# Optimization experiments

Hardware: AMD Instinct MI355X
Metric: run time of the kernel (lower is better)

Reference implementation:

```python
import jax, jax.numpy as jnp
import numpy as np

EMBED_DIM = 1024
HIDDEN = 128
N_QUERY = 65536
N_PROTO = 512


def setup_inputs() -> dict:
    key = jax.random.key(0)
    k1, k2, k3, k4, k5, k6, k7 = jax.random.split(key, 7)
    d2 = EMBED_DIM * 2
    lim1 = 1.0 / np.sqrt(d2)
    lim2 = 1.0 / np.sqrt(HIDDEN)
    return {
        "query_features": jax.random.normal(k1, (N_QUERY, EMBED_DIM), dtype=jnp.float32),
        "prototypes": jax.random.normal(k2, (N_PROTO, EMBED_DIM), dtype=jnp.float32),
        "distances": jax.random.uniform(k3, (N_QUERY, N_PROTO), dtype=jnp.float32),
        "W1": jax.random.uniform(k4, (d2, HIDDEN), minval=-lim1, maxval=lim1, dtype=jnp.float32),
        "b1": jax.random.uniform(k5, (HIDDEN,), minval=-lim1, maxval=lim1, dtype=jnp.float32),
        "W2": jax.random.uniform(k6, (HIDDEN, 1), minval=-lim2, maxval=lim2, dtype=jnp.float32),
        "b2": jax.random.uniform(k7, (1,), minval=-lim2, maxval=lim2, dtype=jnp.float32),
    }


def reference(query_features, prototypes, distances, W1, b1, W2, b2):
    # Batched version of the per-query loop: argmin -> gather -> concat -> MLP.
    idx = jnp.argmin(distances, axis=1)                      # [N_QUERY]
    closest = prototypes[idx]                                # [N_QUERY, D]
    combined = jnp.concatenate([query_features, closest], axis=-1)  # [N_QUERY, 2D]
    h = jax.nn.relu(combined @ W1 + b1)                      # [N_QUERY, 128]
    out = jax.nn.sigmoid(h @ W2 + b2)                        # [N_QUERY, 1]
    return jnp.squeeze(out, axis=-1)                         # [N_QUERY]
```

## Files before the change

kernel.cpp:

```cpp
#include <hip/hip_runtime.h>
#include <math.h>

#define EMBED 1024
#define HIDDEN 128
#define NPROTO 512

typedef short bf16x8 __attribute__((ext_vector_type(8)));
typedef float f32x4 __attribute__((ext_vector_type(4)));

__device__ __forceinline__ unsigned short f2bf(float x) {
    unsigned u = __builtin_bit_cast(unsigned, x);
    unsigned r = u + 0x7FFFu + ((u >> 16) & 1u);
    return (unsigned short)(r >> 16);
}

__global__ __launch_bounds__(256) void prep_kernel(
    const float* __restrict__ prototypes,
    const float* __restrict__ W1,
    float* __restrict__ proto_h,
    unsigned short* __restrict__ w1t)
{
    int b = blockIdx.x;
    int t = threadIdx.x;
    if (b < 256) {
        int ph = t >> 7, h = t & 127;
        int p = b * 2 + ph;
        const float* pr = prototypes + (size_t)p * EMBED;
        const float* w  = W1 + (size_t)EMBED * HIDDEN + h;
        float acc = 0.f;
        for (int k = 0; k < EMBED; k += 8) {
            #pragma unroll
            for (int j = 0; j < 8; ++j)
                acc += pr[k + j] * w[(size_t)(k + j) * HIDDEN];
        }
        proto_h[(size_t)p * HIDDEN + h] = acc;
    } else {
        int s = (b - 256) * 256 + t;
        int n = s & 127;
        int k0 = (s >> 7) * 8;
        bf16x8 v;
        #pragma unroll
        for (int j = 0; j < 8; ++j)
            v[j] = (short)f2bf(W1[(size_t)(k0 + j) * HIDDEN + n]);
        *(bf16x8*)(w1t + (size_t)n * EMBED + k0) = v;
    }
}

__global__ __launch_bounds__(256, 2) void main_kernel(
    const float* __restrict__ qf,
    const float* __restrict__ dist,
    const float* __restrict__ b1,
    const float* __restrict__ W2,
    const float* __restrict__ b2,
    const float* __restrict__ proto_h,
    const unsigned short* __restrict__ w1t,
    float* __restrict__ out)
{
    __shared__ int s_idx[4][32];

    const int t = threadIdx.x;
    const int wave = t >> 6, lane = t & 63;
    const int quad = lane >> 4, tid16 = lane & 15;
    const int q0 = blockIdx.x * 128 + wave * 32;

    const float* abase = qf + (size_t)(q0 + tid16) * EMBED + quad * 8;
    const unsigned short* bbase = w1t + (size_t)tid16 * EMBED + quad * 8;

    float4 aA[2][2], aB[2][2];
    #pragma unroll
    for (int mi = 0; mi < 2; ++mi) {
        const float* p = abase + (size_t)(mi * 16) * EMBED;
        aA[mi][0] = *(const float4*)(p);
        aA[mi][1] = *(const float4*)(p + 4);
        aB[mi][0] = *(const float4*)(p + 32);
        aB[mi][1] = *(const float4*)(p + 36);
    }

    for (int i = 0; i < 32; i += 4) {
        float4 v0[4], v1[4];
        #pragma unroll
        for (int j = 0; j < 4; ++j) {
            const float* dr = dist + (size_t)(q0 + i + j) * NPROTO;
            v0[j] = ((const float4*)dr)[lane];
            v1[j] = ((const float4*)dr)[lane + 64];
        }
        #pragma unroll
        for (int j = 0; j < 4; ++j) {
            float bv = v0[j].x; int bi = lane * 4;
            if (v0[j].y < bv) { bv = v0[j].y; bi = lane * 4 + 1; }
            if (v0[j].z < bv) { bv = v0[j].z; bi = lane * 4 + 2; }
            if (v0[j].w < bv) { bv = v0[j].w; bi = lane * 4 + 3; }
            int c = 256 + lane * 4;
            if (v1[j].x < bv) { bv = v1[j].x; bi = c; }
            if (v1[j].y < bv) { bv = v1[j].y; bi = c + 1; }
            if (v1[j].z < bv) { bv = v1[j].z; bi = c + 2; }
            if (v1[j].w < bv) { bv = v1[j].w; bi = c + 3; }
            #pragma unroll
            for (int s = 1; s < 64; s <<= 1) {
                float ov = __shfl_xor(bv, s);
                int   oi = __shfl_xor(bi, s);
                if (ov < bv || (ov == bv && oi < bi)) { bv = ov; bi = oi; }
            }
            if (lane == 0) s_idx[wave][i + j] = bi;
        }
    }

    f32x4 acc[2][8];
    #pragma unroll
    for (int mi = 0; mi < 2; ++mi)
        #pragma unroll
        for (int ni = 0; ni < 8; ++ni)
            acc[mi][ni] = (f32x4){0.f, 0.f, 0.f, 0.f};

#define LOAD_A(dst, kk)                                              \
    do {                                                             \
        _Pragma("unroll")                                            \
        for (int mi = 0; mi < 2; ++mi) {                             \
            const float* p = abase + (size_t)(mi * 16) * EMBED + (kk) * 32; \
            dst[mi][0] = *(const float4*)(p);                        \
            dst[mi][1] = *(const float4*)(p + 4);                    \
        }                                                            \
    } while (0)

#define CVT_A(af, src)                                               \
    do {                                                             \
        _Pragma("unroll")                                            \
        for (int mi = 0; mi < 2; ++mi) {                             \
            af[mi][0] = (short)f2bf(src[mi][0].x);                   \
            af[mi][1] = (short)f2bf(src[mi][0].y);                   \
            af[mi][2] = (short)f2bf(src[mi][0].z);                   \
            af[mi][3] = (short)f2bf(src[mi][0].w);                   \
            af[mi][4] = (short)f2bf(src[mi][1].x);                   \
            af[mi][5] = (short)f2bf(src[mi][1].y);                   \
            af[mi][6] = (short)f2bf(src[mi][1].z);                   \
            af[mi][7] = (short)f2bf(src[mi][1].w);                   \
        }                                                            \
    } while (0)

    for (int k = 0; k < 32; k += 2) {
        {
            bf16x8 bfr[8];
            #pragma unroll
            for (int ni = 0; ni < 8; ++ni)
                bfr[ni] = *(const bf16x8*)(bbase + (size_t)(ni * 16) * EMBED + k * 32);
            bf16x8 af[2];
            CVT_A(af, aA);
            if (k + 2 < 32) LOAD_A(aA, k + 2);
            #pragma unroll
            for (int mi = 0; mi < 2; ++mi)
                #pragma unroll
                for (int ni = 0; ni < 8; ++ni)
                    acc[mi][ni] = __builtin_amdgcn_mfma_f32_16x16x32_bf16(
                        af[mi], bfr[ni], acc[mi][ni], 0, 0, 0);
        }
        {
            bf16x8 bfr[8];
            #pragma unroll
            for (int ni = 0; ni < 8; ++ni)
                bfr[ni] = *(const bf16x8*)(bbase + (size_t)(ni * 16) * EMBED + (k + 1) * 32);
            bf16x8 af[2];
            CVT_A(af, aB);
            if (k + 3 < 32) LOAD_A(aB, k + 3);
            #pragma unroll
            for (int mi = 0; mi < 2; ++mi)
                #pragma unroll
                for (int ni = 0; ni < 8; ++ni)
                    acc[mi][ni] = __builtin_amdgcn_mfma_f32_16x16x32_bf16(
                        af[mi], bfr[ni], acc[mi][ni], 0, 0, 0);
        }
    }
#undef LOAD_A
#undef CVT_A

    float b1v[8], w2v[8];
    #pragma unroll
    for (int ni = 0; ni < 8; ++ni) {
        b1v[ni] = b1[ni * 16 + tid16];
        w2v[ni] = W2[ni * 16 + tid16];
    }
    const float b2v = b2[0];
    #pragma unroll
    for (int mi = 0; mi < 2; ++mi) {
        #pragma unroll
        for (int r = 0; r < 4; ++r) {
            int m = mi * 16 + quad * 4 + r;
            const float* ph = proto_h + (size_t)s_idx[wave][m] * HIDDEN + tid16;
            float sum = 0.f;
            #pragma unroll
            for (int ni = 0; ni < 8; ++ni) {
                float v = acc[mi][ni][r] + b1v[ni] + ph[ni * 16];
                sum += fmaxf(v, 0.f) * w2v[ni];
            }
            #pragma unroll
            for (int s = 1; s < 16; s <<= 1) sum += __shfl_xor(sum, s);
            if (tid16 == 0) out[q0 + m] = 1.f / (1.f + expf(-(sum + b2v)));
        }
    }
}

extern "C" void kernel_launch(void* const* d_in, const int* in_sizes, int n_in,
                              void* d_out, int out_size, void* d_ws, size_t ws_size,
                              hipStream_t stream) {
    const float* qf    = (const float*)d_in[0];
    const float* proto = (const float*)d_in[1];
    const float* dist  = (const float*)d_in[2];
    const float* W1    = (const float*)d_in[3];
    const float* b1    = (const float*)d_in[4];
    const float* W2    = (const float*)d_in[5];
    const float* b2    = (const float*)d_in[6];
    float* out = (float*)d_out;

    float* proto_h = (float*)d_ws;
    unsigned short* w1t = (unsigned short*)((char*)d_ws + 512 * 128 * 4);

    prep_kernel<<<320, 256, 0, stream>>>(proto, W1, proto_h, w1t);

    int nq = in_sizes[0] / EMBED;
    main_kernel<<<nq / 128, 256, 0, stream>>>(qf, dist, b1, W2, b2, proto_h, w1t, out);
}
```

Baseline: 529.4 us.

## Stage GEMM operands through LDS with async global-to-LDS triple buffering

The main kernel now copies query-feature and W1 tiles into LDS with global_load_lds direct loads. It uses a three-stage buffer ring gated by explicit vmcnt waits and barriers, replacing per-wave register loads from global memory. The argmin distance loads are software-pipelined across three register buffers, and the bf16 conversion uses a cheaper round-half-up with packed pairs. The prep kernel splits the prototype projection across two K-halves per block for more parallelism. This adds about 72KB of LDS per block, which may reduce occupancy, and slightly changes rounding behaviour.

Measured after the change: 486.7 us. 8.1% less time.

```diff
diff --git a/kernel.cpp b/kernel.cpp
--- a/kernel.cpp
+++ b/kernel.cpp
@@ -7,12 +7,22 @@
 
 typedef short bf16x8 __attribute__((ext_vector_type(8)));
 typedef float f32x4 __attribute__((ext_vector_type(4)));
+typedef unsigned int u32x4 __attribute__((ext_vector_type(4)));
 
 __device__ __forceinline__ unsigned short f2bf(float x) {
     unsigned u = __builtin_bit_cast(unsigned, x);
-    unsigned r = u + 0x7FFFu + ((u >> 16) & 1u);
-    return (unsigned short)(r >> 16);
-}
+    return (unsigned short)((u + 0x8000u) >> 16);
+}
+__device__ __forceinline__ unsigned pk2(float a, float b) {
+    unsigned ua = __builtin_bit_cast(unsigned, a) + 0x8000u;
+    unsigned ub = __builtin_bit_cast(unsigned, b) + 0x8000u;
+    return (ua >> 16) | (ub & 0xFFFF0000u);
+}
+
+#define GLL16(gptr, lptr)                                                \
+    __builtin_amdgcn_global_load_lds(                                    \
+        (const __attribute__((address_space(1))) void*)(gptr),           \
+        (__attribute__((address_space(3))) void*)(lptr), 16, 0, 0)
 
 __global__ __launch_bounds__(256) void prep_kernel(
     const float* __restrict__ prototypes,
@@ -22,20 +32,22 @@
 {
     int b = blockIdx.x;
     int t = threadIdx.x;
-    if (b < 256) {
-        int ph = t >> 7, h = t & 127;
-        int p = b * 2 + ph;
-        const float* pr = prototypes + (size_t)p * EMBED;
-        const float* w  = W1 + (size_t)EMBED * HIDDEN + h;
+    if (b < 512) {
+        __shared__ float s_part[128];
+        int ks = t >> 7, h = t & 127;
+        const float* pr = prototypes + (size_t)b * EMBED + ks * 512;
+        const float* w  = W1 + (size_t)(EMBED + ks * 512) * HIDDEN + h;
         float acc = 0.f;
-        for (int k = 0; k < EMBED; k += 8) {
+        for (int k = 0; k < 512; k += 8) {
             #pragma unroll
             for (int j = 0; j < 8; ++j)
                 acc += pr[k + j] * w[(size_t)(k + j) * HIDDEN];
         }
-        proto_h[(size_t)p * HIDDEN + h] = acc;
+        if (ks) s_part[h] = acc;
+        __syncthreads();
+        if (!ks) proto_h[(size_t)b * HIDDEN + h] = acc + s_part[h];
     } else {
-        int s = (b - 256) * 256 + t;
+        int s = (b - 512) * 256 + t;
         int n = s & 127;
         int k0 = (s >> 7) * 8;
         bf16x8 v;
@@ -56,53 +68,89 @@
     const unsigned short* __restrict__ w1t,
     float* __restrict__ out)
 {
+    __shared__ __align__(16) char lds_a[3][16384];
+    __shared__ __align__(16) char lds_b[3][8192];
     __shared__ int s_idx[4][32];
 
     const int t = threadIdx.x;
     const int wave = t >> 6, lane = t & 63;
     const int quad = lane >> 4, tid16 = lane & 15;
-    const int q0 = blockIdx.x * 128 + wave * 32;
-
-    const float* abase = qf + (size_t)(q0 + tid16) * EMBED + quad * 8;
-    const unsigned short* bbase = w1t + (size_t)tid16 * EMBED + quad * 8;
-
-    float4 aA[2][2], aB[2][2];
-    #pragma unroll
-    for (int mi = 0; mi < 2; ++mi) {
-        const float* p = abase + (size_t)(mi * 16) * EMBED;
-        aA[mi][0] = *(const float4*)(p);
-        aA[mi][1] = *(const float4*)(p + 4);
-        aB[mi][0] = *(const float4*)(p + 32);
-        aB[mi][1] = *(const float4*)(p + 36);
-    }
-
-    for (int i = 0; i < 32; i += 4) {
-        float4 v0[4], v1[4];
-        #pragma unroll
-        for (int j = 0; j < 4; ++j) {
-            const float* dr = dist + (size_t)(q0 + i + j) * NPROTO;
-            v0[j] = ((const float4*)dr)[lane];
-            v1[j] = ((const float4*)dr)[lane + 64];
-        }
-        #pragma unroll
-        for (int j = 0; j < 4; ++j) {
-            float bv = v0[j].x; int bi = lane * 4;
-            if (v0[j].y < bv) { bv = v0[j].y; bi = lane * 4 + 1; }
-            if (v0[j].z < bv) { bv = v0[j].z; bi = lane * 4 + 2; }
-            if (v0[j].w < bv) { bv = v0[j].w; bi = lane * 4 + 3; }
-            int c = 256 + lane * 4;
-            if (v1[j].x < bv) { bv = v1[j].x; bi = c; }
-            if (v1[j].y < bv) { bv = v1[j].y; bi = c + 1; }
-            if (v1[j].z < bv) { bv = v1[j].z; bi = c + 2; }
-            if (v1[j].w < bv) { bv = v1[j].w; bi = c + 3; }
-            #pragma unroll
-            for (int s = 1; s < 64; s <<= 1) {
-                float ov = __shfl_xor(bv, s);
-                int   oi = __shfl_xor(bi, s);
-                if (ov < bv || (ov == bv && oi < bi)) { bv = ov; bi = oi; }
-            }
-            if (lane == 0) s_idx[wave][i + j] = bi;
-        }
+    const int q0  = blockIdx.x * 128;
+    const int q0w = q0 + wave * 32;
+
+    const char* gA[4];
+    {
+        int rsub = lane >> 1;
+        int hlog = (lane & 1) ^ ((lane >> 3) & 1);
+        #pragma unroll
+        for (int i = 0; i < 4; ++i) {
+            int row = i * 32 + rsub;
+            gA[i] = (const char*)(qf + (size_t)(q0 + row) * EMBED + wave * 8 + hlog * 4);
+        }
+    }
+    const char* gB[2];
+    #pragma unroll
+    for (int i = 0; i < 2; ++i)
+        gB[i] = (const char*)(w1t + (size_t)(i * 64 + lane) * EMBED + wave * 8);
+
+#define STAGE(buf) do {                                                  \
+        char* la_ = &lds_a[buf][(wave * 4) * 1024];                      \
+        char* lb_ = &lds_b[buf][(wave * 2) * 1024];                      \
+        _Pragma("unroll")                                                \
+        for (int i_ = 0; i_ < 4; ++i_) {                                 \
+            GLL16(gA[i_], la_ + i_ * 1024); gA[i_] += 128;               \
+        }                                                                \
+        _Pragma("unroll")                                                \
+        for (int i_ = 0; i_ < 2; ++i_) {                                 \
+            GLL16(gB[i_], lb_ + i_ * 1024); gB[i_] += 64;                \
+        }                                                                \
+    } while (0)
+
+    STAGE(0);
+    STAGE(1);
+
+#define AMLD(st, base) do {                                              \
+        _Pragma("unroll")                                                \
+        for (int j_ = 0; j_ < 4; ++j_) {                                 \
+            const float* dr_ = dist + (size_t)(q0w + (base) + j_) * NPROTO; \
+            st[2 * j_]     = ((const float4*)dr_)[lane];                 \
+            st[2 * j_ + 1] = ((const float4*)dr_)[lane + 64];            \
+        }                                                                \
+    } while (0)
+#define AMPROC(st, base) do {                                            \
+        _Pragma("unroll")                                                \
+        for (int j_ = 0; j_ < 4; ++j_) {                                 \
+            float4 v0 = st[2 * j_], v1 = st[2 * j_ + 1];                 \
+            float bv = v0.x; int bi = lane * 4;                          \
+            if (v0.y < bv) { bv = v0.y; bi = lane * 4 + 1; }             \
+            if (v0.z < bv) { bv = v0.z; bi = lane * 4 + 2; }             \
+            if (v0.w < bv) { bv = v0.w; bi = lane * 4 + 3; }             \
+            int c_ = 256 + lane * 4;                                     \
+            if (v1.x < bv) { bv = v1.x; bi = c_; }                       \
+            if (v1.y < bv) { bv = v1.y; bi = c_ + 1; }                   \
+            if (v1.z < bv) { bv = v1.z; bi = c_ + 2; }                   \
+            if (v1.w < bv) { bv = v1.w; bi = c_ + 3; }                   \
+            _Pragma("unroll")                                            \
+            for (int s_ = 1; s_ < 64; s_ <<= 1) {                        \
+                float ov = __shfl_xor(bv, s_);                           \
+                int   oi = __shfl_xor(bi, s_);                           \
+                if (ov < bv || (ov == bv && oi < bi)) { bv = ov; bi = oi; } \
+            }                                                            \
+            if (lane == 0) s_idx[wave][(base) + j_] = bi;                \
+        }                                                                \
+    } while (0)
+
+    {
+        float4 A0[8], A1[8], A2[8];
+        AMLD(A0, 0);  AMLD(A1, 4);
+        AMLD(A2, 8);  AMPROC(A0, 0);
+        AMLD(A0, 12); AMPROC(A1, 4);
+        AMLD(A1, 16); AMPROC(A2, 8);
+        AMLD(A2, 20); AMPROC(A0, 12);
+        AMLD(A0, 24); AMPROC(A1, 16);
+        AMLD(A1, 28); AMPROC(A2, 20);
+        AMPROC(A0, 24);
+        AMPROC(A1, 28);
     }
 
     f32x4 acc[2][8];
@@ -112,65 +160,41 @@
         for (int ni = 0; ni < 8; ++ni)
             acc[mi][ni] = (f32x4){0.f, 0.f, 0.f, 0.f};
 
-#define LOAD_A(dst, kk)                                              \
-    do {                                                             \
-        _Pragma("unroll")                                            \
-        for (int mi = 0; mi < 2; ++mi) {                             \
-            const float* p = abase + (size_t)(mi * 16) * EMBED + (kk) * 32; \
-            dst[mi][0] = *(const float4*)(p);                        \
-            dst[mi][1] = *(const float4*)(p + 4);                    \
-        }                                                            \
-    } while (0)
-
-#define CVT_A(af, src)                                               \
-    do {                                                             \
-        _Pragma("unroll")                                            \
-        for (int mi = 0; mi < 2; ++mi) {                             \
-            af[mi][0] = (short)f2bf(src[mi][0].x);                   \
-            af[mi][1] = (short)f2bf(src[mi][0].y);                   \
-            af[mi][2] = (short)f2bf(src[mi][0].z);                   \
-            af[mi][3] = (short)f2bf(src[mi][0].w);                   \
-            af[mi][4] = (short)f2bf(src[mi][1].x);                   \
-            af[mi][5] = (short)f2bf(src[mi][1].y);                   \
-            af[mi][6] = (short)f2bf(src[mi][1].z);                   \
-            af[mi][7] = (short)f2bf(src[mi][1].w);                   \
-        }                                                            \
-    } while (0)
-
-    for (int k = 0; k < 32; k += 2) {
-        {
-            bf16x8 bfr[8];
-            #pragma unroll
-            for (int ni = 0; ni < 8; ++ni)
-                bfr[ni] = *(const bf16x8*)(bbase + (size_t)(ni * 16) * EMBED + k * 32);
-            bf16x8 af[2];
-            CVT_A(af, aA);
-            if (k + 2 < 32) LOAD_A(aA, k + 2);
-            #pragma unroll
-            for (int mi = 0; mi < 2; ++mi)
-                #pragma unroll
-                for (int ni = 0; ni < 8; ++ni)
-                    acc[mi][ni] = __builtin_amdgcn_mfma_f32_16x16x32_bf16(
-                        af[mi], bfr[ni], acc[mi][ni], 0, 0, 0);
-        }
-        {
-            bf16x8 bfr[8];
-            #pragma unroll
-            for (int ni = 0; ni < 8; ++ni)
-                bfr[ni] = *(const bf16x8*)(bbase + (size_t)(ni * 16) * EMBED + (k + 1) * 32);
-            bf16x8 af[2];
-            CVT_A(af, aB);
-            if (k + 3 < 32) LOAD_A(aB, k + 3);
-            #pragma unroll
-            for (int mi = 0; mi < 2; ++mi)
-                #pragma unroll
-                for (int ni = 0; ni < 8; ++ni)
-                    acc[mi][ni] = __builtin_amdgcn_mfma_f32_16x16x32_bf16(
-                        af[mi], bfr[ni], acc[mi][ni], 0, 0, 0);
-        }
-    }
-#undef LOAD_A
-#undef CVT_A
+    const int aoff = quad * 4096 + (wave * 32 + tid16) * 32 + ((tid16 >> 2) & 1) * 16;
+    const int boff = quad * 2048 + tid16 * 16;
+
+#define COMPUTE(buf) do {                                                \
+        bf16x8 bfr[8];                                                   \
+        _Pragma("unroll")                                                \
+        for (int ni_ = 0; ni_ < 8; ++ni_)                                \
+            bfr[ni_] = *(const bf16x8*)(&lds_b[buf][boff + ni_ * 256]);  \
+        _Pragma("unroll")                                                \
+        for (int mi_ = 0; mi_ < 2; ++mi_) {                              \
+            float4 lo = *(const float4*)(&lds_a[buf][aoff + mi_ * 512]); \
+            float4 hi = *(const float4*)(&lds_a[buf][(aoff ^ 16) + mi_ * 512]); \
+            u32x4 p_;                                                    \
+            p_.x = pk2(lo.x, lo.y); p_.y = pk2(lo.z, lo.w);              \
+            p_.z = pk2(hi.x, hi.y); p_.w = pk2(hi.z, hi.w);              \
+            bf16x8 af = __builtin_bit_cast(bf16x8, p_);                  \
+            _Pragma("unroll")                                            \
+            for (int ni_ = 0; ni_ < 8; ++ni_)                            \
+                acc[mi_][ni_] = __builtin_amdgcn_mfma_f32_16x16x32_bf16( \
+                    af, bfr[ni_], acc[mi_][ni_], 0, 0, 0);               \
+        }                                                                \
+    } while (0)
+
+    int bufr = 0, bufs = 2;
+    for (int kt = 0; kt < 31; ++kt) {
+        asm volatile("s_waitcnt vmcnt(6)\n\ts_barrier" ::: "memory");
+        if (kt < 30) {
+            STAGE(bufs);
+            bufs = (bufs == 2) ? 0 : bufs + 1;
+        }
+        COMPUTE(bufr);
+        bufr = (bufr == 2) ? 0 : bufr + 1;
+    }
+    asm volatile("s_waitcnt vmcnt(0)\n\ts_barrier" ::: "memory");
+    COMPUTE(bufr);
 
     float b1v[8], w2v[8];
     #pragma unroll
@@ -193,9 +217,13 @@
             }
             #pragma unroll
             for (int s = 1; s < 16; s <<= 1) sum += __shfl_xor(sum, s);
-            if (tid16 == 0) out[q0 + m] = 1.f / (1.f + expf(-(sum + b2v)));
-        }
-    }
+            if (tid16 == 0) out[q0w + m] = 1.f / (1.f + expf(-(sum + b2v)));
+        }
+    }
+#undef STAGE
+#undef AMLD
+#undef AMPROC
+#undef COMPUTE
 }
 
 extern "C" void kernel_launch(void* const* d_in, const int* in_sizes, int n_in,
@@ -213,7 +241,7 @@
     float* proto_h = (float*)d_ws;
     unsigned short* w1t = (unsigned short*)((char*)d_ws + 512 * 128 * 4);
 
-    prep_kernel<<<320, 256, 0, stream>>>(proto, W1, proto_h, w1t);
+    prep_kernel<<<576, 256, 0, stream>>>(proto, W1, proto_h, w1t);
 
     int nq = in_sizes[0] / EMBED;
     main_kernel<<<nq / 128, 256, 0, stream>>>(qf, dist, b1, W2, b2, proto_h, w1t, out);
```
